# Optimization experiments

Measured on AMD Instinct MI355X. Metric: run time of the kernel, lower is better.

The kernel has to match this reference:

```python
import jax, jax.numpy as jnp
import numpy as np

BN_EPS = 1e-5


def setup_inputs() -> dict:
    key = jax.random.key(0)
    ks = jax.random.split(key, 6)
    B, C, N, K, T, O = 8, 64, 4096, 20, 3, 64
    feat = jax.random.normal(ks[0], (B, C, N), dtype=jnp.float32)
    idx = jax.random.randint(ks[1], (B, N, K), 0, N, dtype=jnp.int32)
    group_pc = jax.random.normal(ks[2], (B, 3, N, K), dtype=jnp.float32)
    weights = jax.random.normal(ks[3], (B, 20, T, N, K), dtype=jnp.float32) * 0.05
    conv_w = jax.random.normal(ks[4], (O, C * T, K), dtype=jnp.float32) * 0.02
    gamma = jnp.ones((O,), dtype=jnp.float32)
    beta = jnp.zeros((O,), dtype=jnp.float32)
    return {"feat": feat, "idx": idx, "group_pc": group_pc, "weights": weights,
            "conv_w": conv_w, "gamma": gamma, "beta": beta}


def _poly_terms(group_pc):
    # group_pc: (B, 3, N, K) -> 20 Taylor terms (B, 20, N, K)
    X, Y, Z = group_pc[:, 0], group_pc[:, 1], group_pc[:, 2]
    XX, YY, ZZ = X * X, Y * Y, Z * Z
    XY, XZ, YZ = X * Y, X * Z, Y * Z
    ones = jnp.ones_like(X)
    return jnp.stack([
        ones, X, Y, Z,
        XX, YY, ZZ,
        XX * X, YY * Y, ZZ * Z,
        XY, XZ, YZ,
        X * XY, X * XZ, Y * YZ, Y * XY, Z * XZ, Z * YZ, XY * Z,
    ], axis=1)


def reference(feat, idx, group_pc, weights, conv_w, gamma, beta):
    B, C, N = feat.shape
    K = idx.shape[-1]
    T = weights.shape[2]
    # KNN gather: group_feat[b, c, n, j] = feat[b, c, idx[b, n, j]]  -> (B, C, N, K)
    group_feat = jax.vmap(lambda f, i: f[:, i])(feat, idx)
    # 20 polynomial basis terms of XYZ: (B, 20, N, K)
    terms = _poly_terms(group_pc)
    # taylor[b, t, n, k] = sum_p weights[b, p, t, n, k] * terms[b, p, n, k]
    taylor = jnp.einsum('bptnk,bpnk->btnk', weights, terms)
    # Fused outer-product + [1, K] conv (output width 1, no bias since bn=True):
    # out[b, o, n] = sum_{c, t, k} group_feat[b,c,n,k] * taylor[b,t,n,k] * W[o, c*T+t, k]
    w = conv_w.reshape(conv_w.shape[0], C, T, K)
    out = jnp.einsum('bcnk,btnk,octk->bon', group_feat, taylor, w)
    # BatchNorm (training-mode batch stats over B and N) + ReLU
    mean = jnp.mean(out, axis=(0, 2), keepdims=True)
    var = jnp.var(out, axis=(0, 2), keepdims=True)
    out = gamma[None, :, None] * (out - mean) / jnp.sqrt(var + BN_EPS) + beta[None, :, None]
    return jax.nn.relu(out)
```

## Files before the change

kernel.cpp:

```cpp
#include <hip/hip_runtime.h>
#include <hip/hip_bf16.h>

#define B_ 8
#define C_ 64
#define N_ 4096
#define K_ 20
#define T_ 3
#define O_ 64
#define P_ 20
#define NK_ (N_ * K_)
#define BN_EPS 1e-5f
#define KG 5

#define WS_FEATH 0
#define WS_WT (WS_FEATH + 1048576)
#define WS_RAW (WS_WT + 122880)
#define WS_PART (WS_RAW + B_ * O_ * N_)
#define WS_STATS (WS_PART + 131072)

typedef __attribute__((ext_vector_type(8))) _Float16 half8;
typedef __attribute__((ext_vector_type(2))) _Float16 half2v;
typedef __attribute__((ext_vector_type(2))) __fp16 fp16x2;
typedef __attribute__((ext_vector_type(16))) float f32x16;

union UH8 {
    uint4 u;
    half8 h;
    half2v h2[4];
};
union UH2 {
    unsigned u;
    half2v h;
    fp16x2 f;
};

__device__ inline unsigned cvt_pkrtz_u(float a, float b) {
    UH2 x;
    x.f = __builtin_amdgcn_cvt_pkrtz(a, b);
    return x.u;
}

__global__ void k_transpose_feat(const float* __restrict__ feat,
                                 unsigned short* __restrict__ featH) {
    __shared__ float t[64][65];
    int bid = blockIdx.x;
    int b = bid & 7;
    int n0 = (bid >> 3) << 6;
    int lx = threadIdx.x & 63, ly = threadIdx.x >> 6;
    const float* fp = feat + b * C_ * N_;
#pragma unroll
    for (int cc = 0; cc < 16; ++cc) {
        int c = ly * 16 + cc;
        t[c][lx] = fp[c * N_ + n0 + lx];
    }
    __syncthreads();
    unsigned short* op = featH + (size_t)(b * N_ + n0) * C_;
#pragma unroll
    for (int u = 0; u < 16; ++u) {
        int n = ly * 16 + u;
        op[n * C_ + lx] = (unsigned short)(cvt_pkrtz_u(t[lx][n], 0.f) & 0xffffu);
    }
}

__global__ void k_pack_w(const float* __restrict__ cw, _Float16* __restrict__ Wh) {
    int e = blockIdx.x * 256 + threadIdx.x;
    int j = e & 7;
    int l = (e >> 3) & 63;
    int frag = e >> 9;
    int oh = frag & 1;
    int cc = (frag >> 1) & 3;
    int kt = frag >> 3;
    int t = kt % 3, k = kt / 3;
    int o = oh * 32 + (l & 31);
    int c = cc * 16 + (l >> 5) * 8 + j;
    Wh[e] = (_Float16)cw[o * (C_ * T_ * K_) + (c * T_ + t) * K_ + k];
}

__global__ __launch_bounds__(512, 4) void k_main(const unsigned short* __restrict__ featH,
                                                 const _Float16* __restrict__ Wh,
                                                 const float* __restrict__ weights,
                                                 const float* __restrict__ gpc,
                                                 const int* __restrict__ idx,
                                                 float* __restrict__ raw,
                                                 float* __restrict__ part) {
    __shared__ unsigned short E[2][KG][32][68];
    __shared__ union {
        unsigned tayH[T_][K_][32];
        float out[64][36];
    } su;

    const int bid0 = blockIdx.x;
    const int bid = (bid0 & 7) * 128 + (bid0 >> 3);
    const int b = bid >> 7;
    const int n0 = (bid & 127) << 5;
    const int tid = threadIdx.x;
    const int lane = tid & 63;
    const int wv = tid >> 6;
    const int wc = wv & 3;
    const int wo = wv >> 2;
    const int nl = lane & 31;
    const int kf = lane >> 5;
    const int row = tid >> 4, seg = tid & 15;

    const unsigned short* fbH = featH + (size_t)b * N_ * C_;

    unsigned idxp[10];
    {
        const int4* ip4 = (const int4*)(idx + (size_t)(b * N_ + n0 + row) * K_);
#pragma unroll
        for (int q = 0; q < 5; ++q) {
            int4 v = ip4[q];
            idxp[q * 2 + 0] = (unsigned)v.x | ((unsigned)v.y << 16);
            idxp[q * 2 + 1] = (unsigned)v.z | ((unsigned)v.w << 16);
        }
    }
#define IDXAT(kidx) ((idxp[(kidx) >> 1] >> (((kidx)&1) * 16)) & 0xffffu)

    uint2 gA[KG];
#pragma unroll
    for (int kk = 0; kk < KG; ++kk)
        gA[kk] = *(const uint2*)(fbH + (size_t)IDXAT(kk) * C_ + seg * 4);

    {
        const float* gpcb = gpc + (size_t)b * 3 * NK_ + n0 * K_;
        const float* wb0 = weights + (size_t)b * P_ * T_ * NK_ + n0 * K_;
        for (int e = tid; e < 32 * K_; e += 512) {
            float X = gpcb[e];
            float Y = gpcb[NK_ + e];
            float Z = gpcb[2 * NK_ + e];
            float XX = X * X, YY = Y * Y, ZZ = Z * Z;
            float XY = X * Y, XZ = X * Z, YZ = Y * Z;
            float terms[20];
            terms[0] = 1.f; terms[1] = X;      terms[2] = Y;       terms[3] = Z;
            terms[4] = XX;  terms[5] = YY;     terms[6] = ZZ;
            terms[7] = XX * X; terms[8] = YY * Y; terms[9] = ZZ * Z;
            terms[10] = XY; terms[11] = XZ;    terms[12] = YZ;
            terms[13] = X * XY;
            terms[14] = X * XZ;
            terms[15] = Y * YZ;
            terms[16] = Y * XY;
            terms[17] = Z * XZ;
            terms[18] = Z * YZ;
            terms[19] = XY * Z;
            float a0 = 0.f, a1 = 0.f, a2 = 0.f;
            const float* wp = wb0 + e;
#pragma unroll
            for (int p = 0; p < P_; ++p) {
                float tp = terms[p];
                a0 += wp[0] * tp;
                a1 += wp[(size_t)NK_] * tp;
                a2 += wp[2 * (size_t)NK_] * tp;
                wp += 3 * (size_t)NK_;
            }
            int n = e / K_, k = e - n * K_;
            su.tayH[0][k][n] = cvt_pkrtz_u(a0, a0);
            su.tayH[1][k][n] = cvt_pkrtz_u(a1, a1);
            su.tayH[2][k][n] = cvt_pkrtz_u(a2, a2);
        }
    }

    f32x16 acc;
#pragma unroll
    for (int i = 0; i < 16; ++i) acc[i] = 0.f;

#pragma unroll
    for (int p = 0; p < 4; ++p) {
#pragma unroll
        for (int kk = 0; kk < KG; ++kk)
            *(uint2*)&E[p & 1][kk][row][seg * 4] = gA[kk];
        if (p + 1 < 4) {
#pragma unroll
            for (int kk = 0; kk < KG; ++kk)
                gA[kk] = *(const uint2*)(fbH + (size_t)IDXAT((p + 1) * KG + kk) * C_ + seg * 4);
        }
        UH8 ar[KG][3];
#pragma unroll
        for (int kk = 0; kk < KG; ++kk)
#pragma unroll
            for (int t = 0; t < 3; ++t)
                ar[kk][t].u = *(const uint4*)(
                    Wh + (size_t)(((((p * KG + kk) * 3 + t) * 4 + wc) * 2 + wo) * 64 + lane) * 8);
#pragma unroll
        for (int kk = 0; kk < KG; ++kk)
#pragma unroll
            for (int t = 0; t < 3; ++t)
                asm volatile("" : "+v"(ar[kk][t].u.x), "+v"(ar[kk][t].u.y),
                                  "+v"(ar[kk][t].u.z), "+v"(ar[kk][t].u.w));
        __syncthreads();
#pragma unroll
        for (int kk = 0; kk < KG; ++kk) {
            UH8 gv;
            gv.u = *(const uint4*)&E[p & 1][kk][nl][wc * 16 + kf * 8];
            const int k = p * KG + kk;
#pragma unroll
            for (int t = 0; t < 3; ++t) {
                UH2 tv;
                tv.u = su.tayH[t][k][nl];
                UH8 bv;
#pragma unroll
                for (int i = 0; i < 4; ++i) bv.h2[i] = gv.h2[i] * tv.h;
                acc = __builtin_amdgcn_mfma_f32_32x32x16_f16(ar[kk][t].h, bv.h, acc, 0, 0, 0);
            }
        }
    }

    __syncthreads();
#pragma unroll 1
    for (int ww = 0; ww < 4; ++ww) {
        if (wc == ww) {
#pragma unroll
            for (int rr = 0; rr < 16; ++rr) {
                int orow = wo * 32 + (rr & 3) + ((rr >> 2) << 3) + (kf << 2);
                if (ww == 0)
                    su.out[orow][nl] = acc[rr];
                else
                    su.out[orow][nl] += acc[rr];
            }
        }
        __syncthreads();
    }

    {
        int o = tid >> 3, sg = tid & 7;
        float4* dst = (float4*)(raw + ((b * O_ + o) * N_) + n0 + sg * 4);
        const float* srow = &su.out[o][sg * 4];
        *dst = make_float4(srow[0], srow[1], srow[2], srow[3]);
    }
    if (tid < 64) {
        float s1 = 0.f, s2 = 0.f;
#pragma unroll 8
        for (int n = 0; n < 32; ++n) {
            float v = su.out[tid][n];
            s1 += v;
            s2 += v * v;
        }
        part[(bid * 64 + tid) * 2 + 0] = s1;
        part[(bid * 64 + tid) * 2 + 1] = s2;
    }
}

__global__ void k_bnstats(const float* __restrict__ part, const float* __restrict__ gamma,
                          const float* __restrict__ beta, float* __restrict__ stats) {
    int o = blockIdx.x;
    int tid = threadIdx.x;
    __shared__ float s1s[256], s2s[256];
    float s1 = 0.f, s2 = 0.f;
    for (int j = tid; j < 1024; j += 256) {
        s1 += part[(j * 64 + o) * 2 + 0];
        s2 += part[(j * 64 + o) * 2 + 1];
    }
    s1s[tid] = s1;
    s2s[tid] = s2;
    __syncthreads();
    for (int s = 128; s > 0; s >>= 1) {
        if (tid < s) {
            s1s[tid] += s1s[tid + s];
            s2s[tid] += s2s[tid + s];
        }
        __syncthreads();
    }
    if (tid == 0) {
        const float cnt = (float)(B_ * N_);
        float mean = s1s[0] / cnt;
        float var = s2s[0] / cnt - mean * mean;
        float sc = gamma[o] * rsqrtf(var + BN_EPS);
        stats[o * 2 + 0] = sc;
        stats[o * 2 + 1] = beta[o] - mean * sc;
    }
}

__global__ void k_finalize(const float* __restrict__ raw, const float* __restrict__ stats,
                           float* __restrict__ out) {
    int e = (blockIdx.x * 256 + threadIdx.x) * 4;
    int o = (e >> 12) & 63;
    float sc = stats[o * 2 + 0], sh = stats[o * 2 + 1];
    float4 v = *(const float4*)(raw + e);
    v.x = fmaxf(v.x * sc + sh, 0.f);
    v.y = fmaxf(v.y * sc + sh, 0.f);
    v.z = fmaxf(v.z * sc + sh, 0.f);
    v.w = fmaxf(v.w * sc + sh, 0.f);
    *(float4*)(out + e) = v;
}

extern "C" void kernel_launch(void* const* d_in, const int* in_sizes, int n_in,
                              void* d_out, int out_size, void* d_ws, size_t ws_size,
                              hipStream_t stream) {
    const float* feat = (const float*)d_in[0];
    const int* idx = (const int*)d_in[1];
    const float* gpc = (const float*)d_in[2];
    const float* weights = (const float*)d_in[3];
    const float* conv_w = (const float*)d_in[4];
    const float* gamma = (const float*)d_in[5];
    const float* beta = (const float*)d_in[6];
    float* out = (float*)d_out;
    float* ws = (float*)d_ws;

    unsigned short* featH = (unsigned short*)(ws + WS_FEATH);
    _Float16* Wh = (_Float16*)(ws + WS_WT);
    float* raw = ws + WS_RAW;
    float* part = ws + WS_PART;
    float* stats = ws + WS_STATS;

    hipLaunchKernelGGL(k_transpose_feat, dim3(512), dim3(256), 0, stream, feat, featH);
    hipLaunchKernelGGL(k_pack_w, dim3((K_ * T_ * C_ * O_) / 256), dim3(256), 0, stream, conv_w,
                       Wh);
    hipLaunchKernelGGL(k_main, dim3(B_ * (N_ / 32)), dim3(512), 0, stream, featH, Wh, weights,
                       gpc, idx, raw, part);
    hipLaunchKernelGGL(k_bnstats, dim3(O_), dim3(256), 0, stream, part, gamma, beta, stats);
    hipLaunchKernelGGL(k_finalize, dim3(B_ * O_ * N_ / 4 / 256), dim3(256), 0, stream, raw, stats,
                       out);
}
```

Measured before the change: 76.49 us.

## Double tile to 64 points per block, sharing conv-weight fragments across two MFMA tiles

Each block now covers 64 points instead of 32 and issues two MFMAs per weight fragment, so every packed conv-weight load from global memory feeds twice as much work and the block count halves. The gather pipeline is restructured to 5 stages of 4 neighbours, with two register sets prefetching two stages ahead and barriers that wait only on LDS counters. The Taylor coefficients move to separate 16-bit LDS storage, while the gather buffer and the output buffer share one union. Register and LDS pressure rise, which may lower occupancy, and there are fewer blocks for the GPU to spread across its units.

Result: slower. 103.7 us (+35.5%).

```diff
diff --git a/kernel.cpp b/kernel.cpp
--- a/kernel.cpp
+++ b/kernel.cpp
@@ -10,13 +10,13 @@
 #define P_ 20
 #define NK_ (N_ * K_)
 #define BN_EPS 1e-5f
-#define KG 5
+#define KG 4
 
 #define WS_FEATH 0
 #define WS_WT (WS_FEATH + 1048576)
 #define WS_RAW (WS_WT + 122880)
 #define WS_PART (WS_RAW + B_ * O_ * N_)
-#define WS_STATS (WS_PART + 131072)
+#define WS_STATS (WS_PART + 65536)
 
 typedef __attribute__((ext_vector_type(8))) _Float16 half8;
 typedef __attribute__((ext_vector_type(2))) _Float16 half2v;
@@ -39,6 +39,12 @@
     x.f = __builtin_amdgcn_cvt_pkrtz(a, b);
     return x.u;
 }
+
+#define LGKM_BARRIER()                                      \
+    do {                                                    \
+        asm volatile("s_waitcnt lgkmcnt(0)" ::: "memory");  \
+        __builtin_amdgcn_s_barrier();                       \
+    } while (0)
 
 __global__ void k_transpose_feat(const float* __restrict__ feat,
                                  unsigned short* __restrict__ featH) {
@@ -83,16 +89,16 @@
                                                  const int* __restrict__ idx,
                                                  float* __restrict__ raw,
                                                  float* __restrict__ part) {
-    __shared__ unsigned short E[2][KG][32][68];
     __shared__ union {
-        unsigned tayH[T_][K_][32];
-        float out[64][36];
+        unsigned short E[2][KG][64][68];
+        float out[64][68];
     } su;
+    __shared__ unsigned short tayS[T_][K_][64];
 
     const int bid0 = blockIdx.x;
-    const int bid = (bid0 & 7) * 128 + (bid0 >> 3);
-    const int b = bid >> 7;
-    const int n0 = (bid & 127) << 5;
+    const int bid = (bid0 & 7) * 64 + (bid0 >> 3);
+    const int b = bid >> 6;
+    const int n0 = (bid & 63) << 6;
     const int tid = threadIdx.x;
     const int lane = tid & 63;
     const int wv = tid >> 6;
@@ -100,31 +106,42 @@
     const int wo = wv >> 2;
     const int nl = lane & 31;
     const int kf = lane >> 5;
-    const int row = tid >> 4, seg = tid & 15;
+    const int r1 = tid >> 4, r2 = r1 + 32, seg = tid & 15;
 
     const unsigned short* fbH = featH + (size_t)b * N_ * C_;
 
-    unsigned idxp[10];
+    unsigned idxp1[10], idxp2[10];
     {
-        const int4* ip4 = (const int4*)(idx + (size_t)(b * N_ + n0 + row) * K_);
+        const int4* ip1 = (const int4*)(idx + (size_t)(b * N_ + n0 + r1) * K_);
+        const int4* ip2 = (const int4*)(idx + (size_t)(b * N_ + n0 + r2) * K_);
 #pragma unroll
         for (int q = 0; q < 5; ++q) {
-            int4 v = ip4[q];
-            idxp[q * 2 + 0] = (unsigned)v.x | ((unsigned)v.y << 16);
-            idxp[q * 2 + 1] = (unsigned)v.z | ((unsigned)v.w << 16);
-        }
-    }
-#define IDXAT(kidx) ((idxp[(kidx) >> 1] >> (((kidx)&1) * 16)) & 0xffffu)
-
-    uint2 gA[KG];
-#pragma unroll
-    for (int kk = 0; kk < KG; ++kk)
-        gA[kk] = *(const uint2*)(fbH + (size_t)IDXAT(kk) * C_ + seg * 4);
+            int4 v1 = ip1[q], v2 = ip2[q];
+            idxp1[q * 2 + 0] = (unsigned)v1.x | ((unsigned)v1.y << 16);
+            idxp1[q * 2 + 1] = (unsigned)v1.z | ((unsigned)v1.w << 16);
+            idxp2[q * 2 + 0] = (unsigned)v2.x | ((unsigned)v2.y << 16);
+            idxp2[q * 2 + 1] = (unsigned)v2.z | ((unsigned)v2.w << 16);
+        }
+    }
+#define IDX1(kidx) ((idxp1[(kidx) >> 1] >> (((kidx)&1) * 16)) & 0xffffu)
+#define IDX2(kidx) ((idxp2[(kidx) >> 1] >> (((kidx)&1) * 16)) & 0xffffu)
+
+    uint2 gA[2 * KG], gB[2 * KG];
+#pragma unroll
+    for (int kk = 0; kk < KG; ++kk) {
+        gA[2 * kk + 0] = *(const uint2*)(fbH + (size_t)IDX1(kk) * C_ + seg * 4);
+        gA[2 * kk + 1] = *(const uint2*)(fbH + (size_t)IDX2(kk) * C_ + seg * 4);
+    }
+#pragma unroll
+    for (int kk = 0; kk < KG; ++kk) {
+        gB[2 * kk + 0] = *(const uint2*)(fbH + (size_t)IDX1(KG + kk) * C_ + seg * 4);
+        gB[2 * kk + 1] = *(const uint2*)(fbH + (size_t)IDX2(KG + kk) * C_ + seg * 4);
+    }
 
     {
         const float* gpcb = gpc + (size_t)b * 3 * NK_ + n0 * K_;
         const float* wb0 = weights + (size_t)b * P_ * T_ * NK_ + n0 * K_;
-        for (int e = tid; e < 32 * K_; e += 512) {
+        for (int e = tid; e < 64 * K_; e += 512) {
             float X = gpcb[e];
             float Y = gpcb[NK_ + e];
             float Z = gpcb[2 * NK_ + e];
@@ -153,55 +170,75 @@
                 wp += 3 * (size_t)NK_;
             }
             int n = e / K_, k = e - n * K_;
-            su.tayH[0][k][n] = cvt_pkrtz_u(a0, a0);
-            su.tayH[1][k][n] = cvt_pkrtz_u(a1, a1);
-            su.tayH[2][k][n] = cvt_pkrtz_u(a2, a2);
-        }
-    }
-
-    f32x16 acc;
-#pragma unroll
-    for (int i = 0; i < 16; ++i) acc[i] = 0.f;
-
-#pragma unroll
-    for (int p = 0; p < 4; ++p) {
-#pragma unroll
-        for (int kk = 0; kk < KG; ++kk)
-            *(uint2*)&E[p & 1][kk][row][seg * 4] = gA[kk];
-        if (p + 1 < 4) {
-#pragma unroll
-            for (int kk = 0; kk < KG; ++kk)
-                gA[kk] = *(const uint2*)(fbH + (size_t)IDXAT((p + 1) * KG + kk) * C_ + seg * 4);
-        }
-        UH8 ar[KG][3];
-#pragma unroll
-        for (int kk = 0; kk < KG; ++kk)
-#pragma unroll
-            for (int t = 0; t < 3; ++t)
-                ar[kk][t].u = *(const uint4*)(
-                    Wh + (size_t)(((((p * KG + kk) * 3 + t) * 4 + wc) * 2 + wo) * 64 + lane) * 8);
-#pragma unroll
-        for (int kk = 0; kk < KG; ++kk)
-#pragma unroll
-            for (int t = 0; t < 3; ++t)
-                asm volatile("" : "+v"(ar[kk][t].u.x), "+v"(ar[kk][t].u.y),
-                                  "+v"(ar[kk][t].u.z), "+v"(ar[kk][t].u.w));
-        __syncthreads();
+            tayS[0][k][n] = (unsigned short)(cvt_pkrtz_u(a0, a0) & 0xffffu);
+            tayS[1][k][n] = (unsigned short)(cvt_pkrtz_u(a1, a1) & 0xffffu);
+            tayS[2][k][n] = (unsigned short)(cvt_pkrtz_u(a2, a2) & 0xffffu);
+        }
+    }
+
+#pragma unroll
+    for (int kk = 0; kk < KG; ++kk) {
+        *(uint2*)&su.E[0][kk][r1][seg * 4] = gA[2 * kk + 0];
+        *(uint2*)&su.E[0][kk][r2][seg * 4] = gA[2 * kk + 1];
+    }
+    LGKM_BARRIER();
+
+    f32x16 acc[2];
+#pragma unroll
+    for (int nh = 0; nh < 2; ++nh)
+#pragma unroll
+        for (int i = 0; i < 16; ++i) acc[nh][i] = 0.f;
+
+#pragma unroll
+    for (int p = 0; p < 5; ++p) {
+        if (p + 1 < 5) {
+#pragma unroll
+            for (int kk = 0; kk < KG; ++kk) {
+                uint2 v0 = (p & 1) ? gA[2 * kk + 0] : gB[2 * kk + 0];
+                uint2 v1 = (p & 1) ? gA[2 * kk + 1] : gB[2 * kk + 1];
+                *(uint2*)&su.E[(p + 1) & 1][kk][r1][seg * 4] = v0;
+                *(uint2*)&su.E[(p + 1) & 1][kk][r2][seg * 4] = v1;
+            }
+        }
+        if (p + 2 < 5) {
+#pragma unroll
+            for (int kk = 0; kk < KG; ++kk) {
+                uint2 v0 = *(const uint2*)(fbH + (size_t)IDX1((p + 2) * KG + kk) * C_ + seg * 4);
+                uint2 v1 = *(const uint2*)(fbH + (size_t)IDX2((p + 2) * KG + kk) * C_ + seg * 4);
+                if (p & 1) {
+                    gB[2 * kk + 0] = v0; gB[2 * kk + 1] = v1;
+                } else {
+                    gA[2 * kk + 0] = v0; gA[2 * kk + 1] = v1;
+                }
+            }
+        }
 #pragma unroll
         for (int kk = 0; kk < KG; ++kk) {
-            UH8 gv;
-            gv.u = *(const uint4*)&E[p & 1][kk][nl][wc * 16 + kf * 8];
+            UH8 gv0, gv1;
+            gv0.u = *(const uint4*)&su.E[p & 1][kk][nl][wc * 16 + kf * 8];
+            gv1.u = *(const uint4*)&su.E[p & 1][kk][nl + 32][wc * 16 + kf * 8];
             const int k = p * KG + kk;
 #pragma unroll
             for (int t = 0; t < 3; ++t) {
-                UH2 tv;
-                tv.u = su.tayH[t][k][nl];
-                UH8 bv;
-#pragma unroll
-                for (int i = 0; i < 4; ++i) bv.h2[i] = gv.h2[i] * tv.h;
-                acc = __builtin_amdgcn_mfma_f32_32x32x16_f16(ar[kk][t].h, bv.h, acc, 0, 0, 0);
+                UH8 ar;
+                ar.u = *(const uint4*)(Wh +
+                                       (size_t)((((k * 3 + t) * 4 + wc) * 2 + wo) * 64 + lane) * 8);
+                unsigned tu0 = tayS[t][k][nl];
+                unsigned tu1 = tayS[t][k][nl + 32];
+                UH2 tv0, tv1;
+                tv0.u = tu0 | (tu0 << 16);
+                tv1.u = tu1 | (tu1 << 16);
+                UH8 bv0, bv1;
+#pragma unroll
+                for (int i = 0; i < 4; ++i) {
+                    bv0.h2[i] = gv0.h2[i] * tv0.h;
+                    bv1.h2[i] = gv1.h2[i] * tv1.h;
+                }
+                acc[0] = __builtin_amdgcn_mfma_f32_32x32x16_f16(ar.h, bv0.h, acc[0], 0, 0, 0);
+                acc[1] = __builtin_amdgcn_mfma_f32_32x32x16_f16(ar.h, bv1.h, acc[1], 0, 0, 0);
             }
         }
+        LGKM_BARRIER();
     }
 
     __syncthreads();
@@ -209,27 +246,34 @@
     for (int ww = 0; ww < 4; ++ww) {
         if (wc == ww) {
 #pragma unroll
-            for (int rr = 0; rr < 16; ++rr) {
-                int orow = wo * 32 + (rr & 3) + ((rr >> 2) << 3) + (kf << 2);
-                if (ww == 0)
-                    su.out[orow][nl] = acc[rr];
-                else
-                    su.out[orow][nl] += acc[rr];
-            }
+            for (int nh = 0; nh < 2; ++nh)
+#pragma unroll
+                for (int rr = 0; rr < 16; ++rr) {
+                    int orow = wo * 32 + (rr & 3) + ((rr >> 2) << 3) + (kf << 2);
+                    int col = nh * 32 + nl;
+                    if (ww == 0)
+                        su.out[orow][col] = acc[nh][rr];
+                    else
+                        su.out[orow][col] += acc[nh][rr];
+                }
         }
         __syncthreads();
     }
 
     {
         int o = tid >> 3, sg = tid & 7;
-        float4* dst = (float4*)(raw + ((b * O_ + o) * N_) + n0 + sg * 4);
-        const float* srow = &su.out[o][sg * 4];
-        *dst = make_float4(srow[0], srow[1], srow[2], srow[3]);
+        float4* dst0 = (float4*)(raw + ((b * O_ + o) * N_) + n0 + sg * 4);
+        float4* dst1 = (float4*)(raw + ((b * O_ + o) * N_) + n0 + 32 + sg * 4);
+        const float* srow = &su.out[o][0];
+        *dst0 = make_float4(srow[sg * 4 + 0], srow[sg * 4 + 1], srow[sg * 4 + 2],
+                            srow[sg * 4 + 3]);
+        *dst1 = make_float4(srow[32 + sg * 4 + 0], srow[32 + sg * 4 + 1],
+                            srow[32 + sg * 4 + 2], srow[32 + sg * 4 + 3]);
     }
     if (tid < 64) {
         float s1 = 0.f, s2 = 0.f;
 #pragma unroll 8
-        for (int n = 0; n < 32; ++n) {
+        for (int n = 0; n < 64; ++n) {
             float v = su.out[tid][n];
             s1 += v;
             s2 += v * v;
@@ -245,7 +289,7 @@
     int tid = threadIdx.x;
     __shared__ float s1s[256], s2s[256];
     float s1 = 0.f, s2 = 0.f;
-    for (int j = tid; j < 1024; j += 256) {
+    for (int j = tid; j < 512; j += 256) {
         s1 += part[(j * 64 + o) * 2 + 0];
         s2 += part[(j * 64 + o) * 2 + 1];
     }
@@ -304,7 +348,7 @@
     hipLaunchKernelGGL(k_transpose_feat, dim3(512), dim3(256), 0, stream, feat, featH);
     hipLaunchKernelGGL(k_pack_w, dim3((K_ * T_ * C_ * O_) / 256), dim3(256), 0, stream, conv_w,
                        Wh);
-    hipLaunchKernelGGL(k_main, dim3(B_ * (N_ / 32)), dim3(512), 0, stream, featH, Wh, weights,
+    hipLaunchKernelGGL(k_main, dim3(B_ * (N_ / 64)), dim3(512), 0, stream, featH, Wh, weights,
                        gpc, idx, raw, part);
     hipLaunchKernelGGL(k_bnstats, dim3(O_), dim3(256), 0, stream, part, gamma, beta, stats);
     hipLaunchKernelGGL(k_finalize, dim3(B_ * O_ * N_ / 4 / 256), dim3(256), 0, stream, raw, stats,
```

## Deepen gather prefetch to two stages and load weights inline per MFMA

Applied to the files above, without the earlier changes.

Restructures the main loop so neighbor-feature gathers are issued two stages ahead into alternating register buffers, with the LDS staging write moved after the MFMAs of the current stage and a single barrier per iteration. Weight fragments are now loaded right before each MFMA instead of being batched per stage with an asm register pin. Indices are kept as full ints instead of packed 16-bit pairs. The aim is to hide gather latency behind compute and reduce register pressure, at the cost of more live registers for the second gather buffer and weight loads sitting closer to their use.

Result: faster. 71.65 us (-6.3%).

```diff
diff --git a/kernel.cpp b/kernel.cpp
--- a/kernel.cpp
+++ b/kernel.cpp
@@ -104,22 +104,23 @@
 
     const unsigned short* fbH = featH + (size_t)b * N_ * C_;
 
-    unsigned idxp[10];
+    int idxv[K_];
     {
         const int4* ip4 = (const int4*)(idx + (size_t)(b * N_ + n0 + row) * K_);
 #pragma unroll
         for (int q = 0; q < 5; ++q) {
             int4 v = ip4[q];
-            idxp[q * 2 + 0] = (unsigned)v.x | ((unsigned)v.y << 16);
-            idxp[q * 2 + 1] = (unsigned)v.z | ((unsigned)v.w << 16);
-        }
-    }
-#define IDXAT(kidx) ((idxp[(kidx) >> 1] >> (((kidx)&1) * 16)) & 0xffffu)
-
-    uint2 gA[KG];
+            idxv[q * 4 + 0] = v.x;
+            idxv[q * 4 + 1] = v.y;
+            idxv[q * 4 + 2] = v.z;
+            idxv[q * 4 + 3] = v.w;
+        }
+    }
+
+    uint2 gA[KG], gB[KG];
 #pragma unroll
     for (int kk = 0; kk < KG; ++kk)
-        gA[kk] = *(const uint2*)(fbH + (size_t)IDXAT(kk) * C_ + seg * 4);
+        gA[kk] = *(const uint2*)(fbH + (size_t)idxv[kk] * C_ + seg * 4);
 
     {
         const float* gpcb = gpc + (size_t)b * 3 * NK_ + n0 * K_;
@@ -159,34 +160,27 @@
         }
     }
 
+#pragma unroll
+    for (int kk = 0; kk < KG; ++kk)
+        *(uint2*)&E[0][kk][row][seg * 4] = gA[kk];
+#pragma unroll
+    for (int kk = 0; kk < KG; ++kk)
+        gA[kk] = *(const uint2*)(fbH + (size_t)idxv[KG + kk] * C_ + seg * 4);
+    __syncthreads();
+
     f32x16 acc;
 #pragma unroll
     for (int i = 0; i < 16; ++i) acc[i] = 0.f;
 
 #pragma unroll
     for (int p = 0; p < 4; ++p) {
-#pragma unroll
-        for (int kk = 0; kk < KG; ++kk)
-            *(uint2*)&E[p & 1][kk][row][seg * 4] = gA[kk];
-        if (p + 1 < 4) {
-#pragma unroll
-            for (int kk = 0; kk < KG; ++kk)
-                gA[kk] = *(const uint2*)(fbH + (size_t)IDXAT((p + 1) * KG + kk) * C_ + seg * 4);
-        }
-        UH8 ar[KG][3];
-#pragma unroll
-        for (int kk = 0; kk < KG; ++kk)
-#pragma unroll
-            for (int t = 0; t < 3; ++t)
-                ar[kk][t].u = *(const uint4*)(
-                    Wh + (size_t)(((((p * KG + kk) * 3 + t) * 4 + wc) * 2 + wo) * 64 + lane) * 8);
-#pragma unroll
-        for (int kk = 0; kk < KG; ++kk)
-#pragma unroll
-            for (int t = 0; t < 3; ++t)
-                asm volatile("" : "+v"(ar[kk][t].u.x), "+v"(ar[kk][t].u.y),
-                                  "+v"(ar[kk][t].u.z), "+v"(ar[kk][t].u.w));
-        __syncthreads();
+        if (p + 2 < 4) {
+#pragma unroll
+            for (int kk = 0; kk < KG; ++kk) {
+                uint2 v = *(const uint2*)(fbH + (size_t)idxv[(p + 2) * KG + kk] * C_ + seg * 4);
+                if (p & 1) gA[kk] = v; else gB[kk] = v;
+            }
+        }
 #pragma unroll
         for (int kk = 0; kk < KG; ++kk) {
             UH8 gv;
@@ -194,17 +188,27 @@
             const int k = p * KG + kk;
 #pragma unroll
             for (int t = 0; t < 3; ++t) {
+                UH8 ar;
+                ar.u = *(const uint4*)(Wh +
+                                       (size_t)((((k * 3 + t) * 4 + wc) * 2 + wo) * 64 + lane) * 8);
                 UH2 tv;
                 tv.u = su.tayH[t][k][nl];
                 UH8 bv;
 #pragma unroll
                 for (int i = 0; i < 4; ++i) bv.h2[i] = gv.h2[i] * tv.h;
-                acc = __builtin_amdgcn_mfma_f32_32x32x16_f16(ar[kk][t].h, bv.h, acc, 0, 0, 0);
-            }
-        }
-    }
-
-    __syncthreads();
+                acc = __builtin_amdgcn_mfma_f32_32x32x16_f16(ar.h, bv.h, acc, 0, 0, 0);
+            }
+        }
+        if (p + 1 < 4) {
+#pragma unroll
+            for (int kk = 0; kk < KG; ++kk) {
+                uint2 v = (p & 1) ? gB[kk] : gA[kk];
+                *(uint2*)&E[(p + 1) & 1][kk][row][seg * 4] = v;
+            }
+        }
+        __syncthreads();
+    }
+
 #pragma unroll 1
     for (int ww = 0; ww < 4; ++ww) {
         if (wc == ww) {
```
